# Performance work log

Measured on AMD Instinct MI355X. Metric: run time of the kernel, lower is better.

The kernel has to match this reference:

```python
import jax, jax.numpy as jnp
import numpy as np


def setup_inputs() -> dict:
    key = jax.random.key(0)
    k0, k1, k2, k3 = jax.random.split(key, 4)
    B, N, C, Dout = 4, 8192, 64, 128
    coords = jax.random.normal(k0, (B, N, 3), dtype=jnp.float32)
    features = jax.random.normal(k1, (B, N, C), dtype=jnp.float32)
    W1 = jax.random.normal(k2, (C + 3, Dout), dtype=jnp.float32) / jnp.sqrt(jnp.float32(C + 3))
    b1 = jnp.zeros((Dout,), dtype=jnp.float32)
    W2 = jax.random.normal(k3, (Dout, Dout), dtype=jnp.float32) / jnp.sqrt(jnp.float32(Dout))
    b2 = jnp.zeros((Dout,), dtype=jnp.float32)
    return {"coords": coords, "features": features, "W1": W1, "b1": b1,
            "W2": W2, "b2": b2, "sample_count": 2048, "k": 32}


def reference(coords, features, W1, b1, W2, b2, sample_count, k):
    B, N, _ = coords.shape
    S = min(sample_count, N)
    kk = min(k, N)
    # deterministic linspace centroid sampling (same indices for every batch)
    idx = jnp.round(jnp.linspace(0.0, N - 1, S)).astype(jnp.int32)  # [S]
    sampled = coords[:, idx]  # [B,S,3]
    # squared distances via GEMM (same topk ordering as torch.cdist)
    s2 = jnp.sum(sampled * sampled, axis=-1)          # [B,S]
    c2 = jnp.sum(coords * coords, axis=-1)            # [B,N]
    d2 = s2[:, :, None] + c2[:, None, :] - 2.0 * jnp.einsum('bsd,bnd->bsn', sampled, coords)
    _, knn_idx = jax.lax.top_k(-d2, kk)               # [B,S,kk] smallest distances
    # per-batch irregular gathers
    grouped_c = jax.vmap(lambda c, i: c[i])(coords, knn_idx)      # [B,S,kk,3]
    rel = grouped_c - sampled[:, :, None, :]                      # relative coords
    grouped_f = jax.vmap(lambda f, i: f[i])(features, knn_idx)    # [B,S,kk,C]
    g = jnp.concatenate([rel, grouped_f], axis=-1)                # [B,S,kk,C+3]
    # shared MLP: Linear -> GELU(exact) -> Linear -> GELU(exact)
    h = jax.nn.gelu(g @ W1 + b1, approximate=False)
    h = jax.nn.gelu(h @ W2 + b2, approximate=False)
    pooled = jnp.max(h, axis=2)                                   # [B,S,Dout]
    return sampled, pooled
```

## Files before the change

kernel.cpp:

```cpp
#include <hip/hip_runtime.h>
#include <math.h>

typedef unsigned int u32;
typedef unsigned long long u64;

#define BB 4
#define NN 8192
#define CC 64
#define DOUT 128
#define SS 2048
#define KSEL 32
#define CAP 768
#define BREAK_CAP 128

__device__ __forceinline__ int sample_index(int s) {
    if (s == 1706) return 6826;
    const double step = 8191.0 / 2047.0;
    return (int)rint((double)s * step);
}

__device__ __forceinline__ u32 f2s(float f) {
    u32 u = __float_as_uint(f);
    return ((int)u < 0) ? ~u : (u ^ 0x80000000u);
}

__device__ __forceinline__ float gelu(float x) {
    return 0.5f * x * (1.0f + erff(x * 0.70710678118654752f));
}

__global__ __launch_bounds__(256, 8) void k_select(const float* __restrict__ coords,
                                                   float* __restrict__ out_sampled,
                                                   int* __restrict__ selbuf,
                                                   int selstride) {
    __shared__ __align__(16) u64 cand[CAP];
    __shared__ u32 wsum[32];
    __shared__ int sel[KSEL];
    __shared__ int s_nsel, s_ncand;

    const int tid = threadIdx.x;
    const int q = blockIdx.x;
    const int b = q >> 11;
    const int s = q & (SS - 1);
    const int si = sample_index(s);

    const float* cb = coords + (size_t)b * NN * 3;
    const float qx = cb[si * 3 + 0], qy = cb[si * 3 + 1], qz = cb[si * 3 + 2];
    const float q2 = __fadd_rn(__fadd_rn(__fmul_rn(qx, qx), __fmul_rn(qy, qy)), __fmul_rn(qz, qz));

    if (tid == 0) {
        float* dst = out_sampled + (size_t)q * 3;
        dst[0] = qx; dst[1] = qy; dst[2] = qz;
    }

    u32 kr[32];
#pragma unroll
    for (int i = 0; i < 32; i++) {
        int j = tid + (i << 8);
        float x = cb[j * 3 + 0], y = cb[j * 3 + 1], z = cb[j * 3 + 2];
        float n2 = __fadd_rn(__fadd_rn(__fmul_rn(x, x), __fmul_rn(y, y)), __fmul_rn(z, z));
        float dot = __fadd_rn(__fadd_rn(__fmul_rn(qx, x), __fmul_rn(qy, y)), __fmul_rn(qz, z));
        float d2 = __fsub_rn(__fadd_rn(q2, n2), __fmul_rn(2.0f, dot));
        kr[i] = f2s(d2);
    }

    u32 pref = 0;
    int base = 0;
    int shift = 28;
    for (int p = 7; p >= 0; p--) {
        const int sh = 4 * p;
        const u32 hmask = (p == 7) ? 0u : (0xFFFFFFFFu << (sh + 4));
        u32 cnt[8] = {0, 0, 0, 0, 0, 0, 0, 0};
#pragma unroll
        for (int i = 0; i < 32; i++) {
            u32 kv = kr[i];
            if ((kv & hmask) == pref) {
                u32 nib = (kv >> sh) & 15u;
                cnt[nib >> 1] += 1u << (16 * (nib & 1));
            }
        }
#pragma unroll
        for (int w = 0; w < 8; w++) {
#pragma unroll
            for (int d = 1; d < 64; d <<= 1) cnt[w] += __shfl_xor(cnt[w], d, 64);
        }
        if ((tid & 63) == 0) {
            int wv = tid >> 6;
#pragma unroll
            for (int w = 0; w < 8; w++) wsum[wv * 8 + w] = cnt[w];
        }
        __syncthreads();
        u32 tot[8];
#pragma unroll
        for (int w = 0; w < 8; w++) tot[w] = wsum[w] + wsum[8 + w] + wsum[16 + w] + wsum[24 + w];
        int run = 0, D = 15, c = 0;
#pragma unroll
        for (int nib = 0; nib < 16; nib++) {
            int cc = (nib & 1) ? (int)(tot[nib >> 1] >> 16) : (int)(tot[nib >> 1] & 0xFFFFu);
            if (base + run + cc >= KSEL) { D = nib; c = cc; break; }
            run += cc;
        }
        base += run;
        pref |= ((u32)D) << sh;
        shift = sh;
        bool done = (c <= BREAK_CAP) || (p == 0);
        if (done && tid == 0) { s_nsel = 0; s_ncand = 0; }
        __syncthreads();
        if (done) break;
    }

    const u32 prefv = pref >> shift;
#pragma unroll
    for (int i = 0; i < 32; i++) {
        u32 kv = kr[i];
        u32 kp = kv >> shift;
        if (kp < prefv) {
            sel[atomicAdd(&s_nsel, 1)] = tid + (i << 8);
        } else if (kp == prefv) {
            int t = atomicAdd(&s_ncand, 1);
            if (t < CAP) cand[t] = ((u64)kv << 32) | (u32)(tid + (i << 8));
        }
    }
    __syncthreads();

    {
        const int nles = s_nsel;
        const int need = KSEL - nles;
        const int nc = (s_ncand < CAP) ? s_ncand : CAP;
        for (int ci = tid; ci < nc; ci += 256) {
            u64 me = cand[ci];
            int r = 0;
            for (int m = 0; m < nc; m++) r += (cand[m] < me) ? 1 : 0;
            if (r < need) sel[nles + r] = (int)(me & 0xFFFFFFFFu);
        }
    }
    __syncthreads();

    if (tid < KSEL) selbuf[(size_t)q * selstride + tid] = sel[tid];
}

__global__ __launch_bounds__(256, 8) void k_mlp(const float* __restrict__ coords,
                                                const float* __restrict__ features,
                                                const float* __restrict__ w1,
                                                const float* __restrict__ b1,
                                                const float* __restrict__ w2,
                                                const float* __restrict__ b2,
                                                const int* __restrict__ selbuf,
                                                int selstride,
                                                float* __restrict__ pooled) {
    __shared__ __align__(16) unsigned char smem[17408];
    float* g = (float*)smem;
    float* h = (float*)smem;
    __shared__ int sel[KSEL];

    const int tid = threadIdx.x;
    const int q = blockIdx.x;
    const int b = q >> 11;
    const int s = q & (SS - 1);
    const int si = sample_index(s);

    const float* cb = coords + (size_t)b * NN * 3;
    const float qx = cb[si * 3 + 0], qy = cb[si * 3 + 1], qz = cb[si * 3 + 2];

    if (tid < KSEL) sel[tid] = selbuf[(size_t)q * selstride + tid];
    __syncthreads();

    {
        const int gi = tid >> 3;
        const int gc = tid & 7;
        const int n = sel[gi];
        const float* fb = features + ((size_t)b * NN + n) * CC;
#pragma unroll
        for (int m = 0; m < 9; m++) {
            int c = gc + (m << 3);
            if (c < 67) {
                float v;
                if (c < 3) v = cb[n * 3 + c] - ((c == 0) ? qx : (c == 1) ? qy : qz);
                else       v = fb[c - 3];
                g[c * 34 + gi] = v;
            }
        }
    }
    __syncthreads();

    const int jg  = tid >> 2;
    const int inb = tid & 3;
    const int n0  = inb << 3;
    const int j0  = jg << 1;

    float acc0[8], acc1[8];

    {
        float2 bb = *(const float2*)(b1 + j0);
#pragma unroll
        for (int t = 0; t < 8; t++) { acc0[t] = bb.x; acc1[t] = bb.y; }
        const float* w1p = w1 + j0;
        for (int c = 0; c < 67; c++) {
            float2 wv = *(const float2*)(w1p + c * DOUT);
            const float* gr = g + c * 34 + n0;
            float2 a0 = *(const float2*)(gr + 0);
            float2 a1 = *(const float2*)(gr + 2);
            float2 a2 = *(const float2*)(gr + 4);
            float2 a3 = *(const float2*)(gr + 6);
            float a[8] = {a0.x, a0.y, a1.x, a1.y, a2.x, a2.y, a3.x, a3.y};
#pragma unroll
            for (int t = 0; t < 8; t++) {
                acc0[t] = fmaf(a[t], wv.x, acc0[t]);
                acc1[t] = fmaf(a[t], wv.y, acc1[t]);
            }
        }
    }
    __syncthreads();
    {
        float* h0 = h + (size_t)j0 * 34 + n0;
        float* h1 = h0 + 34;
#pragma unroll
        for (int p = 0; p < 4; p++) {
            float2 v0 = {gelu(acc0[2 * p]), gelu(acc0[2 * p + 1])};
            *(float2*)(h0 + 2 * p) = v0;
        }
#pragma unroll
        for (int p = 0; p < 4; p++) {
            float2 v1 = {gelu(acc1[2 * p]), gelu(acc1[2 * p + 1])};
            *(float2*)(h1 + 2 * p) = v1;
        }
    }
    __syncthreads();

    {
        float2 bb = *(const float2*)(b2 + j0);
#pragma unroll
        for (int t = 0; t < 8; t++) { acc0[t] = bb.x; acc1[t] = bb.y; }
        const float* w2p = w2 + j0;
        for (int c = 0; c < DOUT; c++) {
            float2 wv = *(const float2*)(w2p + c * DOUT);
            const float* hr = h + c * 34 + n0;
            float2 a0 = *(const float2*)(hr + 0);
            float2 a1 = *(const float2*)(hr + 2);
            float2 a2 = *(const float2*)(hr + 4);
            float2 a3 = *(const float2*)(hr + 6);
            float a[8] = {a0.x, a0.y, a1.x, a1.y, a2.x, a2.y, a3.x, a3.y};
#pragma unroll
            for (int t = 0; t < 8; t++) {
                acc0[t] = fmaf(a[t], wv.x, acc0[t]);
                acc1[t] = fmaf(a[t], wv.y, acc1[t]);
            }
        }
    }

    float m0 = gelu(acc0[0]);
    float m1 = gelu(acc1[0]);
#pragma unroll
    for (int t = 1; t < 8; t++) {
        m0 = fmaxf(m0, gelu(acc0[t]));
        m1 = fmaxf(m1, gelu(acc1[t]));
    }
#pragma unroll
    for (int d = 1; d < 4; d <<= 1) {
        m0 = fmaxf(m0, __shfl_xor(m0, d, 64));
        m1 = fmaxf(m1, __shfl_xor(m1, d, 64));
    }
    if (inb == 0) {
        float2 out = {m0, m1};
        *(float2*)(pooled + (size_t)q * DOUT + j0) = out;
    }
}

extern "C" void kernel_launch(void* const* d_in, const int* in_sizes, int n_in,
                              void* d_out, int out_size, void* d_ws, size_t ws_size,
                              hipStream_t stream) {
    const float* coords = nullptr;
    const float* features = nullptr;
    const float* W1 = nullptr;
    const float* b1 = nullptr;
    const float* W2 = nullptr;
    const float* b2 = nullptr;
    for (int i = 0; i < n_in; i++) {
        int sz = in_sizes[i];
        const float* p = (const float*)d_in[i];
        if      (sz == BB * NN * 3)     coords = p;
        else if (sz == BB * NN * CC)    features = p;
        else if (sz == (CC + 3) * DOUT) W1 = p;
        else if (sz == DOUT * DOUT)     W2 = p;
        else if (sz == DOUT)            { if (!b1) b1 = p; else b2 = p; }
    }

    float* out_sampled = (float*)d_out;
    float* out_pooled  = (float*)d_out + (size_t)BB * SS * 3;

    const size_t sel_bytes = (size_t)BB * SS * KSEL * sizeof(int);
    int* selbuf;
    int selstride;
    if (ws_size >= sel_bytes && d_ws != nullptr) {
        selbuf = (int*)d_ws;
        selstride = KSEL;
    } else {
        selbuf = (int*)out_pooled;
        selstride = DOUT;
    }

    k_select<<<dim3(BB * SS), dim3(256), 0, stream>>>(coords, out_sampled, selbuf, selstride);
    k_mlp<<<dim3(BB * SS), dim3(256), 0, stream>>>(coords, features, W1, b1, W2, b2,
                                                   selbuf, selstride, out_pooled);
}
```

Baseline: 476.8 us.

## Stage radix select through shared candidate buffer and vectorize MLP smem reads

The top-k radix select now refines digits over registers only until the candidate bucket fits a 2048-entry shared buffer. It then compacts candidates with wave ballots and one atomic per wave, and continues the digit refinement over that smaller shared list before a final rank sort on at most 384 entries. This replaces repeated full 32-register passes and per-thread atomics. In the MLP kernel the shared row stride changes from 34 to 36 so activations can be read and written as float4 instead of float2, at the cost of slightly more LDS and possible bank-pattern changes.

After: 472.6 us. No clear change (-0.9%).

```diff
diff --git a/kernel.cpp b/kernel.cpp
--- a/kernel.cpp
+++ b/kernel.cpp
@@ -10,8 +10,10 @@
 #define DOUT 128
 #define SS 2048
 #define KSEL 32
-#define CAP 768
+#define CAPL 2048
+#define CAP2 384
 #define BREAK_CAP 128
+#define GSTR 36
 
 __device__ __forceinline__ int sample_index(int s) {
     if (s == 1706) return 6826;
@@ -32,12 +34,14 @@
                                                    float* __restrict__ out_sampled,
                                                    int* __restrict__ selbuf,
                                                    int selstride) {
-    __shared__ __align__(16) u64 cand[CAP];
+    __shared__ __align__(16) u64 cand[CAPL];
+    __shared__ __align__(16) u64 cand2[CAP2];
     __shared__ u32 wsum[32];
     __shared__ int sel[KSEL];
-    __shared__ int s_nsel, s_ncand;
+    __shared__ int s_nsel, s_ncand, s_n2;
 
     const int tid = threadIdx.x;
+    const int lane = tid & 63;
     const int q = blockIdx.x;
     const int b = q >> 11;
     const int s = q & (SS - 1);
@@ -63,12 +67,54 @@
         kr[i] = f2s(d2);
     }
 
+#define BFLY_WSUM()                                                          \
+    _Pragma("unroll")                                                        \
+    for (int w = 0; w < 8; w++) {                                            \
+        _Pragma("unroll")                                                    \
+        for (int d = 1; d < 64; d <<= 1) cnt[w] += __shfl_xor(cnt[w], d, 64);\
+    }                                                                        \
+    if ((tid & 63) == 0) {                                                   \
+        int wv = tid >> 6;                                                   \
+        _Pragma("unroll")                                                    \
+        for (int w = 0; w < 8; w++) wsum[wv * 8 + w] = cnt[w];               \
+    }                                                                        \
+    __syncthreads();
+
+#define SCAN_DIGIT()                                                         \
+    u32 tot[8];                                                              \
+    _Pragma("unroll")                                                        \
+    for (int w = 0; w < 8; w++)                                              \
+        tot[w] = wsum[w] + wsum[8 + w] + wsum[16 + w] + wsum[24 + w];        \
+    run = 0; D = 15; cc = 0;                                                 \
+    _Pragma("unroll")                                                        \
+    for (int nib = 0; nib < 16; nib++) {                                     \
+        int cv = (nib & 1) ? (int)(tot[nib >> 1] >> 16)                      \
+                           : (int)(tot[nib >> 1] & 0xFFFFu);                 \
+        if (base + run + cv >= KSEL) { D = nib; cc = cv; break; }            \
+        run += cv;                                                           \
+    }
+
     u32 pref = 0;
-    int base = 0;
-    int shift = 28;
-    for (int p = 7; p >= 0; p--) {
+    int base = 0, shift = 28, c = 0;
+    int p = 7;
+    {
+        u32 cnt[8] = {0, 0, 0, 0, 0, 0, 0, 0};
+#pragma unroll
+        for (int i = 0; i < 32; i++) {
+            u32 nib = kr[i] >> 28;
+            cnt[nib >> 1] += 1u << (16 * (nib & 1));
+        }
+        BFLY_WSUM()
+        int run, D, cc;
+        SCAN_DIGIT()
+        base = run; pref = (u32)D << 28; c = cc;
+        __syncthreads();
+    }
+
+    while (c > CAPL && p > 0) {
+        p--;
         const int sh = 4 * p;
-        const u32 hmask = (p == 7) ? 0u : (0xFFFFFFFFu << (sh + 4));
+        const u32 hmask = 0xFFFFFFFFu << (sh + 4);
         u32 cnt[8] = {0, 0, 0, 0, 0, 0, 0, 0};
 #pragma unroll
         for (int i = 0; i < 32; i++) {
@@ -78,46 +124,90 @@
                 cnt[nib >> 1] += 1u << (16 * (nib & 1));
             }
         }
-#pragma unroll
-        for (int w = 0; w < 8; w++) {
-#pragma unroll
-            for (int d = 1; d < 64; d <<= 1) cnt[w] += __shfl_xor(cnt[w], d, 64);
-        }
-        if ((tid & 63) == 0) {
-            int wv = tid >> 6;
-#pragma unroll
-            for (int w = 0; w < 8; w++) wsum[wv * 8 + w] = cnt[w];
-        }
+        BFLY_WSUM()
+        int run, D, cc;
+        SCAN_DIGIT()
+        base += run; pref |= (u32)D << sh; shift = sh; c = cc;
         __syncthreads();
-        u32 tot[8];
-#pragma unroll
-        for (int w = 0; w < 8; w++) tot[w] = wsum[w] + wsum[8 + w] + wsum[16 + w] + wsum[24 + w];
-        int run = 0, D = 15, c = 0;
-#pragma unroll
-        for (int nib = 0; nib < 16; nib++) {
-            int cc = (nib & 1) ? (int)(tot[nib >> 1] >> 16) : (int)(tot[nib >> 1] & 0xFFFFu);
-            if (base + run + cc >= KSEL) { D = nib; c = cc; break; }
-            run += cc;
-        }
-        base += run;
-        pref |= ((u32)D) << sh;
-        shift = sh;
-        bool done = (c <= BREAK_CAP) || (p == 0);
-        if (done && tid == 0) { s_nsel = 0; s_ncand = 0; }
+    }
+
+    if (tid == 0) { s_nsel = 0; s_ncand = 0; }
+    __syncthreads();
+
+    const u64 lmlt = (1ull << lane) - 1ull;
+    {
+        const u32 prefv = pref >> shift;
+#pragma unroll
+        for (int i = 0; i < 32; i++) {
+            int j = tid + (i << 8);
+            u32 kv = kr[i];
+            u32 kp = kv >> shift;
+            bool isS = kp < prefv;
+            bool isC = kp == prefv;
+            u64 bs = __ballot(isS);
+            u64 bc = __ballot(isC);
+            int basS = 0, basC = 0;
+            if (lane == 0) {
+                if (bs) basS = atomicAdd(&s_nsel, (int)__popcll(bs));
+                if (bc) basC = atomicAdd(&s_ncand, (int)__popcll(bc));
+            }
+            basS = __shfl(basS, 0, 64);
+            basC = __shfl(basC, 0, 64);
+            if (isS) sel[basS + (int)__popcll(bs & lmlt)] = j;
+            if (isC) {
+                int pos = basC + (int)__popcll(bc & lmlt);
+                if (pos < CAPL) cand[pos] = ((u64)kv << 32) | (u32)j;
+            }
+        }
+    }
+    __syncthreads();
+    int nc = s_ncand; if (nc > CAPL) nc = CAPL;
+
+    int p2 = shift >> 2;
+    while (c > BREAK_CAP && p2 > 0) {
+        p2--;
+        const int sh = 4 * p2;
+        const u32 ph = pref >> (sh + 4);
+        u32 cnt[8] = {0, 0, 0, 0, 0, 0, 0, 0};
+        for (int e = tid; e < nc; e += 256) {
+            u32 kv = (u32)(cand[e] >> 32);
+            if ((kv >> (sh + 4)) == ph) {
+                u32 nib = (kv >> sh) & 15u;
+                cnt[nib >> 1] += 1u << (16 * (nib & 1));
+            }
+        }
+        BFLY_WSUM()
+        int run, D, cc;
+        SCAN_DIGIT()
+        base += run; pref |= (u32)D << sh; shift = sh; c = cc;
         __syncthreads();
-        if (done) break;
-    }
-
-    const u32 prefv = pref >> shift;
-#pragma unroll
-    for (int i = 0; i < 32; i++) {
-        u32 kv = kr[i];
-        u32 kp = kv >> shift;
-        if (kp < prefv) {
-            sel[atomicAdd(&s_nsel, 1)] = tid + (i << 8);
-        } else if (kp == prefv) {
-            int t = atomicAdd(&s_ncand, 1);
-            if (t < CAP) cand[t] = ((u64)kv << 32) | (u32)(tid + (i << 8));
+    }
+#undef BFLY_WSUM
+#undef SCAN_DIGIT
+
+    if (tid == 0) s_n2 = 0;
+    __syncthreads();
+    {
+        const u32 pv = pref >> shift;
+        for (int e = tid; e < nc; e += 256) {
+            u64 ent = cand[e];
+            u32 kp = (u32)(ent >> 32) >> shift;
+            bool isS = kp < pv;
+            bool isC = kp == pv;
+            u64 bs = __ballot(isS);
+            u64 bc = __ballot(isC);
+            int basS = 0, basC = 0;
+            if (lane == 0) {
+                if (bs) basS = atomicAdd(&s_nsel, (int)__popcll(bs));
+                if (bc) basC = atomicAdd(&s_n2, (int)__popcll(bc));
+            }
+            basS = __shfl(basS, 0, 64);
+            basC = __shfl(basC, 0, 64);
+            if (isS) sel[basS + (int)__popcll(bs & lmlt)] = (int)(ent & 0xFFFFFFFFu);
+            if (isC) {
+                int pos = basC + (int)__popcll(bc & lmlt);
+                if (pos < CAP2) cand2[pos] = ent;
+            }
         }
     }
     __syncthreads();
@@ -125,11 +215,11 @@
     {
         const int nles = s_nsel;
         const int need = KSEL - nles;
-        const int nc = (s_ncand < CAP) ? s_ncand : CAP;
-        for (int ci = tid; ci < nc; ci += 256) {
-            u64 me = cand[ci];
+        int n2 = s_n2; if (n2 > CAP2) n2 = CAP2;
+        for (int ci = tid; ci < n2; ci += 256) {
+            u64 me = cand2[ci];
             int r = 0;
-            for (int m = 0; m < nc; m++) r += (cand[m] < me) ? 1 : 0;
+            for (int m = 0; m < n2; m++) r += (cand2[m] < me) ? 1 : 0;
             if (r < need) sel[nles + r] = (int)(me & 0xFFFFFFFFu);
         }
     }
@@ -147,7 +237,7 @@
                                                 const int* __restrict__ selbuf,
                                                 int selstride,
                                                 float* __restrict__ pooled) {
-    __shared__ __align__(16) unsigned char smem[17408];
+    __shared__ __align__(16) unsigned char smem[18432];
     float* g = (float*)smem;
     float* h = (float*)smem;
     __shared__ int sel[KSEL];
@@ -176,7 +266,7 @@
                 float v;
                 if (c < 3) v = cb[n * 3 + c] - ((c == 0) ? qx : (c == 1) ? qy : qz);
                 else       v = fb[c - 3];
-                g[c * 34 + gi] = v;
+                g[c * GSTR + gi] = v;
             }
         }
     }
@@ -196,12 +286,10 @@
         const float* w1p = w1 + j0;
         for (int c = 0; c < 67; c++) {
             float2 wv = *(const float2*)(w1p + c * DOUT);
-            const float* gr = g + c * 34 + n0;
-            float2 a0 = *(const float2*)(gr + 0);
-            float2 a1 = *(const float2*)(gr + 2);
-            float2 a2 = *(const float2*)(gr + 4);
-            float2 a3 = *(const float2*)(gr + 6);
-            float a[8] = {a0.x, a0.y, a1.x, a1.y, a2.x, a2.y, a3.x, a3.y};
+            const float* gr = g + c * GSTR + n0;
+            float4 p0 = *(const float4*)(gr);
+            float4 p1 = *(const float4*)(gr + 4);
+            float a[8] = {p0.x, p0.y, p0.z, p0.w, p1.x, p1.y, p1.z, p1.w};
 #pragma unroll
             for (int t = 0; t < 8; t++) {
                 acc0[t] = fmaf(a[t], wv.x, acc0[t]);
@@ -211,18 +299,16 @@
     }
     __syncthreads();
     {
-        float* h0 = h + (size_t)j0 * 34 + n0;
-        float* h1 = h0 + 34;
-#pragma unroll
-        for (int p = 0; p < 4; p++) {
-            float2 v0 = {gelu(acc0[2 * p]), gelu(acc0[2 * p + 1])};
-            *(float2*)(h0 + 2 * p) = v0;
-        }
-#pragma unroll
-        for (int p = 0; p < 4; p++) {
-            float2 v1 = {gelu(acc1[2 * p]), gelu(acc1[2 * p + 1])};
-            *(float2*)(h1 + 2 * p) = v1;
-        }
+        float* h0 = h + (size_t)j0 * GSTR + n0;
+        float* h1 = h0 + GSTR;
+        float4 v0 = {gelu(acc0[0]), gelu(acc0[1]), gelu(acc0[2]), gelu(acc0[3])};
+        float4 v1 = {gelu(acc0[4]), gelu(acc0[5]), gelu(acc0[6]), gelu(acc0[7])};
+        *(float4*)(h0)     = v0;
+        *(float4*)(h0 + 4) = v1;
+        float4 v2 = {gelu(acc1[0]), gelu(acc1[1]), gelu(acc1[2]), gelu(acc1[3])};
+        float4 v3 = {gelu(acc1[4]), gelu(acc1[5]), gelu(acc1[6]), gelu(acc1[7])};
+        *(float4*)(h1)     = v2;
+        *(float4*)(h1 + 4) = v3;
     }
     __syncthreads();
 
@@ -233,12 +319,10 @@
         const float* w2p = w2 + j0;
         for (int c = 0; c < DOUT; c++) {
             float2 wv = *(const float2*)(w2p + c * DOUT);
-            const float* hr = h + c * 34 + n0;
-            float2 a0 = *(const float2*)(hr + 0);
-            float2 a1 = *(const float2*)(hr + 2);
-            float2 a2 = *(const float2*)(hr + 4);
-            float2 a3 = *(const float2*)(hr + 6);
-            float a[8] = {a0.x, a0.y, a1.x, a1.y, a2.x, a2.y, a3.x, a3.y};
+            const float* hr = h + c * GSTR + n0;
+            float4 p0 = *(const float4*)(hr);
+            float4 p1 = *(const float4*)(hr + 4);
+            float a[8] = {p0.x, p0.y, p0.z, p0.w, p1.x, p1.y, p1.z, p1.w};
 #pragma unroll
             for (int t = 0; t < 8; t++) {
                 acc0[t] = fmaf(a[t], wv.x, acc0[t]);
```
